# Performance work log

Measured on AMD Instinct MI355X. Metric: run time of the kernel, lower is better.

The kernel has to match this reference:

```python
import jax, jax.numpy as jnp
import numpy as np

EPS = 1e-4      # geomloss: eps = blur**p = 0.01**2
N_ITERS = 20    # fixed Sinkhorn iterations
UNI_T = 2.0     # uniformity temperature (Wang & Isola)


def _sqdist(x, y):
    # [N,D],[M,D] -> [N,M] squared euclidean distances
    return jnp.sum((x[:, None, :] - y[None, :, :]) ** 2, axis=-1)


def _cost(x, y):
    # geomloss p=2 cost: ||x-y||^2 / 2
    return 0.5 * _sqdist(x, y)


def _softmin(C, h):
    # f_i = -eps * log( (1/M) * sum_j exp((h_j - C_ij)/eps) )
    M = C.shape[1]
    lse = jax.nn.logsumexp((h[None, :] - C) / EPS, axis=1)
    return -EPS * (lse - jnp.log(jnp.float32(M)))


def _sinkhorn_potentials(C):
    # alternating log-domain Sinkhorn updates, uniform weights
    def body(carry, _):
        f, g = carry
        f = _softmin(C, g)
        g = _softmin(C.T, f)
        return (f, g), None
    init = (jnp.zeros(C.shape[0], C.dtype), jnp.zeros(C.shape[1], C.dtype))
    (f, g), _ = jax.lax.scan(body, init, None, length=N_ITERS)
    return f, g


def _sym_potential(C):
    # symmetric fixed-point for the debiasing terms OT_eps(a,a)
    def body(p, _):
        return 0.5 * (p + _softmin(C, p)), None
    p, _ = jax.lax.scan(body, jnp.zeros(C.shape[0], C.dtype), None, length=N_ITERS)
    return p


def sinkhorn_divergence(x, y):
    # debiased: S = OT(x,y) - 0.5*OT(x,x) - 0.5*OT(y,y); envelope-theorem grads
    Cxy = _cost(x, y)
    f_d, g_d = _sinkhorn_potentials(jax.lax.stop_gradient(Cxy))
    f = _softmin(Cxy, jax.lax.stop_gradient(g_d))          # final differentiable step
    g = _softmin(Cxy.T, jax.lax.stop_gradient(f_d))

    Cxx = _cost(x, x)
    px = _sym_potential(jax.lax.stop_gradient(Cxx))
    fx = _softmin(Cxx, jax.lax.stop_gradient(px))          # 0.5*OT(x,x) = mean(fx)

    Cyy = _cost(y, y)
    py = _sym_potential(jax.lax.stop_gradient(Cyy))
    fy = _softmin(Cyy, jax.lax.stop_gradient(py))

    return jnp.mean(f) + jnp.mean(g) - jnp.mean(fx) - jnp.mean(fy)


def uniformity(x):
    # log E_{i != j} [ exp(-t * ||x_i - x_j||^2) ]
    N = x.shape[0]
    D = _sqdist(x, x)
    D = D + jnp.diag(jnp.full((N,), jnp.inf, dtype=x.dtype))  # mask self-pairs
    return jax.nn.logsumexp(-UNI_T * D) - jnp.log(jnp.float32(N * (N - 1)))


def setup_inputs() -> dict:
    key = jax.random.key(0)
    k1, k2 = jax.random.split(key)
    p_q = jax.random.normal(k1, (4096, 3), dtype=jnp.float32)
    p_gt = jax.random.normal(k2, (4096, 4), dtype=jnp.float32)
    return {"p_q": p_q, "p_gt": p_gt}


def reference(p_q, p_gt):
    L = sinkhorn_divergence(p_q, p_gt[:, :3])
    L = L + uniformity(p_q)
    return L
```

## Files before the change

kernel.cpp:

```cpp
#include <hip/hip_runtime.h>

#define NPT  4096
#define NBLK 256
#define NTHR 1024

constexpr float EPSV   = 1e-4f;
constexpr float LN2F   = 0.69314718055994531f;
constexpr float E2     = EPSV * LN2F;
constexpr float INV_E2 = 1.0f / E2;
constexpr float S_U    = 4.0f / LN2F;

#define SMEM_FLOATS 34816
#define SMEM_BYTES  (SMEM_FLOATS * 4)

typedef float v2f __attribute__((ext_vector_type(2)));

__device__ __forceinline__ float fexp2(float x) { return __builtin_amdgcn_exp2f(x); }
__device__ __forceinline__ float flog2(float x) { return __builtin_amdgcn_logf(x); }

__device__ __forceinline__ v2f pk_fma(v2f a, v2f b, v2f c) {
    v2f d;
    asm("v_pk_fma_f32 %0, %1, %2, %3" : "=v"(d) : "v"(a), "v"(b), "v"(c));
    return d;
}
__device__ __forceinline__ v2f pk_add(v2f a, v2f b) {
    v2f d;
    asm("v_pk_add_f32 %0, %1, %2" : "=v"(d) : "v"(a), "v"(b));
    return d;
}
__device__ __forceinline__ float max3f(float a, float b, float c) {
    float d;
    asm("v_max3_f32 %0, %1, %2, %3" : "=v"(d) : "v"(a), "v"(b), "v"(c));
    return d;
}

template<int CTRL>
__device__ __forceinline__ float dppf(float x) {
    return __int_as_float(__builtin_amdgcn_update_dpp(
        __float_as_int(x), __float_as_int(x), CTRL, 0xF, 0xF, false));
}

__device__ __forceinline__ float gload(const float* p) {
    return __hip_atomic_load(p, __ATOMIC_RELAXED, __HIP_MEMORY_SCOPE_SYSTEM);
}
__device__ __forceinline__ void gstore(float* p, float v) {
    __hip_atomic_store(p, v, __ATOMIC_RELAXED, __HIP_MEMORY_SCOPE_SYSTEM);
}

__device__ __forceinline__ void group_barrier(unsigned* base, unsigned target, int b) {
    asm volatile("s_waitcnt vmcnt(0)" ::: "memory");
    __syncthreads();
    if (threadIdx.x == 0) {
        __hip_atomic_fetch_add(&base[(b & 15) * 16], 1u,
                               __ATOMIC_RELAXED, __HIP_MEMORY_SCOPE_SYSTEM);
        for (;;) {
            unsigned tot = 0;
#pragma unroll
            for (int i = 0; i < 16; ++i)
                tot += __hip_atomic_load(&base[i * 16],
                                         __ATOMIC_RELAXED, __HIP_MEMORY_SCOPE_SYSTEM);
            if (tot >= target) break;
            __builtin_amdgcn_s_sleep(1);
        }
    }
    __syncthreads();
}

template<bool ISU>
__device__ __forceinline__ void run_task(
    const float4* __restrict__ cpA, const float4* __restrict__ cpB,
    const float*  __restrict__ rAf, const float*  __restrict__ rBf,
    int r0g, int half, int lane, float scale, float2* part2, int lr0)
{
    v2f xs0[2], xs1[2], xs2[2];
#pragma unroll
    for (int r = 0; r < 2; ++r) {
        const int rr = r0g + r;
        const int pb4 = (rr >> 1) * 4, c0 = rr & 1;
        float xv = rAf[pb4 + c0] * scale;
        float yv = rAf[pb4 + 2 + c0] * scale;
        float zv = rBf[pb4 + c0] * scale;
        xs0[r] = (v2f){xv, xv};
        xs1[r] = (v2f){yv, yv};
        xs2[r] = (v2f){zv, zv};
    }
    float m[2], s[2];
    const int pbase = half * 1024 + lane;
    const float4* colA = cpA + pbase;
    const float4* colB = cpB + pbase;

#pragma unroll
    for (int chunk = 0; chunk < 4; ++chunk) {
        v2f av[2][4];
        float mc[2] = {-1e30f, -1e30f};
#pragma unroll
        for (int k = 0; k < 4; ++k) {
            const float4 a4 = colA[(chunk * 4 + k) * 64];
            const float4 b4 = colB[(chunk * 4 + k) * 64];
            const v2f xx = {a4.x, a4.y}, yy = {a4.z, a4.w};
            const v2f zz = {b4.x, b4.y}, gg = {b4.z, b4.w};
#pragma unroll
            for (int r = 0; r < 2; ++r) {
                v2f a01 = pk_fma(xs2[r], zz, gg);
                a01 = pk_fma(xs1[r], yy, a01);
                a01 = pk_fma(xs0[r], xx, a01);
                if (ISU) {
                    const int p = pbase + (chunk * 4 + k) * 64;
                    const int rr = r0g + r;
                    if (p == (rr >> 1)) {
                        if (rr & 1) a01.y = -1e30f; else a01.x = -1e30f;
                    }
                }
                av[r][k] = a01;
                mc[r] = max3f(mc[r], a01.x, a01.y);
            }
        }
#pragma unroll
        for (int r = 0; r < 2; ++r) {
            const float nm = -mc[r];
            v2f mcn = {nm, nm};
            float sA = 0.0f, sB = 0.0f;
#pragma unroll
            for (int k = 0; k < 4; ++k) {
                v2f d = pk_add(av[r][k], mcn);
                sA += fexp2(d.x);
                sB += fexp2(d.y);
            }
            const float sc_ = sA + sB;
            if (chunk == 0) { m[r] = mc[r]; s[r] = sc_; }
            else {
                float dd = m[r] - mc[r];
                float e = fexp2(-fabsf(dd));
                float bigs   = (dd >= 0.0f) ? s[r] : sc_;
                float smalls = (dd >= 0.0f) ? sc_  : s[r];
                s[r] = fmaf(smalls, e, bigs);
                m[r] = fmaxf(m[r], mc[r]);
            }
        }
    }
#pragma unroll
    for (int r = 0; r < 2; ++r) {
        const float ml = m[r];
        float mm = m[r];
        mm = fmaxf(mm, dppf<0xB1>(mm));
        mm = fmaxf(mm, dppf<0x4E>(mm));
        mm = fmaxf(mm, dppf<0x141>(mm));
        float ssv = s[r] * fexp2(ml - mm);
        ssv += dppf<0xB1>(ssv);
        ssv += dppf<0x4E>(ssv);
        ssv += dppf<0x141>(ssv);
        if ((lane & 7) == 0)
            part2[(lr0 + r) * 16 + half * 8 + (lane >> 3)] = make_float2(mm, ssv);
    }
}

__global__ void sink_init(float* __restrict__ ws) {
    int t = blockIdx.x * blockDim.x + threadIdx.x;
    if (t < NPT) {
        gstore(ws + t, 0.0f);
        gstore(ws + 4096 + t, 0.0f);
        gstore(ws + 8192 + t, 0.0f);
        gstore(ws + 16384 + t, 0.0f);
    }
    if (t < 512) {
        __hip_atomic_store((unsigned*)(ws + 40960) + t, 0u,
                           __ATOMIC_RELAXED, __HIP_MEMORY_SCOPE_SYSTEM);
    }
}

__global__ __launch_bounds__(NTHR)
__attribute__((amdgpu_waves_per_eu(4, 4)))
void sink_main(
    const float* __restrict__ xin, const float* __restrict__ yin,
    float* __restrict__ ws, float* __restrict__ out)
{
    extern __shared__ float smem[];
    float4* pAx = (float4*)smem;
    float4* pBx = (float4*)(smem + 8192);
    float4* pAy = (float4*)(smem + 16384);
    float4* pBy = (float4*)(smem + 24576);
    float2* part2 = (float2*)(smem + 32768);

    float* f    = ws;
    float* g    = ws + 4096;
    float* px0  = ws + 8192;
    float* px1  = ws + 12288;
    float* py0  = ws + 16384;
    float* py1  = ws + 20480;
    float* ffin = ws + 24576;
    float* fxv  = ws + 28672;
    float* fyv  = ws + 32768;
    float* uls  = ws + 36864;
    unsigned* ctrA = (unsigned*)(ws + 40960);
    unsigned* ctrB = (unsigned*)(ws + 40960) + 256;

    const int tid  = threadIdx.x;
    const int b    = blockIdx.x;
    const int wave = tid >> 6;
    const int lane = tid & 63;
    unsigned* cbarrier = (b < 128) ? ctrA : ctrB;

    const float4* yin4 = (const float4*)yin;
    for (int i = tid; i < 2048; i += NTHR) {
        float x0 = xin[6 * i + 0], y0v = xin[6 * i + 1], z0 = xin[6 * i + 2];
        float x1 = xin[6 * i + 3], y1v = xin[6 * i + 4], z1 = xin[6 * i + 5];
        pAx[i] = make_float4(x0, x1, y0v, y1v);
        pBx[i] = make_float4(z0, z1, 0.0f, 0.0f);
        float4 v0 = yin4[2 * i], v1 = yin4[2 * i + 1];
        pAy[i] = make_float4(v0.x, v1.x, v0.y, v1.y);
        pBy[i] = make_float4(v0.z, v1.z, 0.0f, 0.0f);
    }
    __syncthreads();

    for (int h = 0; h <= 40; ++h) {
        bool rows_x, cols_x, isU = false, avg = false;
        const float* pot; float* outp; float scale = INV_E2;
        int row0g, rows_pb;
        if (h == 0) {
            if (b < 128)      { rows_x = true;  cols_x = false; pot = g;    outp = f;    rows_pb = 32; row0g = b * 32; }
            else if (b < 192) { rows_x = true;  cols_x = true;  pot = px0;  outp = px1;  avg = true; rows_pb = 64; row0g = (b - 128) * 64; }
            else              { rows_x = true;  cols_x = true;  pot = nullptr; outp = uls; isU = true; scale = S_U; rows_pb = 64; row0g = (b - 192) * 64; }
        } else if (h == 40) {
            if (b < 128)      { rows_x = true;  cols_x = false; pot = g;    outp = ffin; rows_pb = 32; row0g = b * 32; }
            else if (b < 192) { rows_x = true;  cols_x = true;  pot = px0;  outp = fxv;  rows_pb = 64; row0g = (b - 128) * 64; }
            else              { rows_x = false; cols_x = false; pot = py0;  outp = fyv;  rows_pb = 64; row0g = (b - 192) * 64; }
        } else if (h & 1) {
            int k = (h - 1) >> 1;
            if (b < 128) { rows_x = false; cols_x = true;  pot = f; outp = g; rows_pb = 32; row0g = b * 32; }
            else         { rows_x = false; cols_x = false; pot = (k & 1) ? py1 : py0; outp = (k & 1) ? py0 : py1; avg = true; rows_pb = 32; row0g = (b - 128) * 32; }
        } else {
            int k = h >> 1;
            if (b < 128) { rows_x = true; cols_x = false; pot = g; outp = f; rows_pb = 32; row0g = b * 32; }
            else         { rows_x = true; cols_x = true;  pot = (k & 1) ? px1 : px0; outp = (k & 1) ? px0 : px1; avg = true; rows_pb = 32; row0g = (b - 128) * 32; }
        }

        float4* cpA = cols_x ? pAx : pAy;
        float4* cpB = cols_x ? pBx : pBy;
        for (int p = tid; p < 2048; p += NTHR) {
            float4 a4 = cpA[p];
            float4 b4 = cpB[p];
            float cn0 = 0.5f * (a4.x * a4.x + a4.z * a4.z + b4.x * b4.x);
            float cn1 = 0.5f * (a4.y * a4.y + a4.w * a4.w + b4.y * b4.y);
            float pv0 = pot ? gload(pot + 2 * p)     : 0.0f;
            float pv1 = pot ? gload(pot + 2 * p + 1) : 0.0f;
            ((float2*)&cpB[p])[1] = make_float2((pv0 - cn0) * scale,
                                                (pv1 - cn1) * scale);
        }
        __syncthreads();

        const float* rAf = (const float*)(rows_x ? pAx : pAy);
        const float* rBf = (const float*)(rows_x ? pBx : pBy);
        const int ntask = rows_pb;
        for (int t = wave; t < ntask; t += 16) {
            int grp = t >> 1, half = t & 1;
            int lr0 = grp << 1;
            int r0g = row0g + lr0;
            if (isU) run_task<true >(cpA, cpB, rAf, rBf, r0g, half, lane, scale, part2, lr0);
            else     run_task<false>(cpA, cpB, rAf, rBf, r0g, half, lane, scale, part2, lr0);
        }
        __syncthreads();

        if (tid < rows_pb) {
            float2 pv2[16];
#pragma unroll
            for (int q = 0; q < 16; ++q) pv2[q] = part2[tid * 16 + q];
            float mm = pv2[0].x;
#pragma unroll
            for (int q = 1; q < 15; q += 2) mm = max3f(mm, pv2[q].x, pv2[q + 1].x);
            mm = fmaxf(mm, pv2[15].x);
            float ss = 0.0f;
#pragma unroll
            for (int q = 0; q < 16; ++q) ss += pv2[q].y * fexp2(pv2[q].x - mm);
            int rg = row0g + tid;
            const int pb4 = (rg >> 1) * 4, c0 = rg & 1;
            float xv = rAf[pb4 + c0];
            float yv = rAf[pb4 + 2 + c0];
            float zv = rBf[pb4 + c0];
            float rn = 0.5f * (xv * xv + yv * yv + zv * zv);
            float lse2 = mm + flog2(ss) - rn * scale;
            float val;
            if (isU) {
                val = lse2;
            } else {
                val = -E2 * (lse2 - 12.0f);
                if (avg) val = 0.5f * (gload(pot + rg) + val);
            }
            gstore(outp + rg, val);
        }

        group_barrier(cbarrier, 128u * (unsigned)(h + 1), b);
    }

    if (b == 0) {
        if (tid == 0) {
            for (;;) {
                unsigned tot = 0;
#pragma unroll
                for (int i = 0; i < 16; ++i)
                    tot += __hip_atomic_load(&ctrB[i * 16],
                                             __ATOMIC_RELAXED, __HIP_MEMORY_SCOPE_SYSTEM);
                if (tot >= 128u * 41u) break;
                __builtin_amdgcn_s_sleep(1);
            }
        }
        __syncthreads();

        float sf = 0.f, sg = 0.f, sx = 0.f, sy = 0.f, um = -1e30f, us = 0.f;
        for (int i = tid; i < NPT; i += NTHR) {
            sf += gload(ffin + i); sg += gload(g + i);
            sx += gload(fxv + i);  sy += gload(fyv + i);
            float v = gload(uls + i);
            float mn = fmaxf(um, v);
            us = us * fexp2(um - mn) + fexp2(v - mn);
            um = mn;
        }
#pragma unroll
        for (int off = 1; off < 64; off <<= 1) {
            sf += __shfl_xor(sf, off, 64);
            sg += __shfl_xor(sg, off, 64);
            sx += __shfl_xor(sx, off, 64);
            sy += __shfl_xor(sy, off, 64);
            float mo = __shfl_xor(um, off, 64);
            float so = __shfl_xor(us, off, 64);
            float mn = fmaxf(um, mo);
            us = us * fexp2(um - mn) + so * fexp2(mo - mn);
            um = mn;
        }
        __syncthreads();
        if (lane == 0) {
            float* red = smem;
            red[wave * 6 + 0] = sf; red[wave * 6 + 1] = sg; red[wave * 6 + 2] = sx;
            red[wave * 6 + 3] = sy; red[wave * 6 + 4] = um; red[wave * 6 + 5] = us;
        }
        __syncthreads();
        if (tid == 0) {
            float* red = smem;
            float Sf = 0, Sg = 0, Sx = 0, Sy = 0, Um = -1e30f, Us = 0;
            for (int w = 0; w < 16; ++w) {
                Sf += red[w * 6 + 0]; Sg += red[w * 6 + 1];
                Sx += red[w * 6 + 2]; Sy += red[w * 6 + 3];
                float mo = red[w * 6 + 4], so = red[w * 6 + 5];
                float mn = fmaxf(Um, mo);
                Us = Us * fexp2(Um - mn) + so * fexp2(mo - mn);
                Um = mn;
            }
            float mean = (Sf + Sg - Sx - Sy) * (1.0f / 4096.0f);
            float U = LN2F * (Um + flog2(Us)) - logf(4096.0f * 4095.0f);
            out[0] = mean + U;
        }
    }
}

extern "C" void kernel_launch(void* const* d_in, const int* in_sizes, int n_in,
                              void* d_out, int out_size, void* d_ws, size_t ws_size,
                              hipStream_t stream) {
    const float* x = (const float*)d_in[0];
    const float* y = (const float*)d_in[1];
    float* ws  = (float*)d_ws;
    float* out = (float*)d_out;

    (void)hipFuncSetAttribute((const void*)sink_main,
                              hipFuncAttributeMaxDynamicSharedMemorySize, SMEM_BYTES);

    sink_init<<<4, 1024, 0, stream>>>(ws);
    sink_main<<<NBLK, NTHR, SMEM_BYTES, stream>>>(x, y, ws, out);
}
```

Before: 533.8 us.

## Use master-release grid barrier and precompute scaled potentials and norms

Replaces the all-blocks-poll grid barrier with a scheme where block 0 of each group polls the counters and publishes a release flag that the other blocks spin on. Adds precomputed squared norms and pre-scaled potential arrays, written by the init kernel and at each step, so the per-step column staging becomes a single 64-bit load instead of a norm recomputation plus two loads. The row norm in the finalize step is now read from a table. The aim is to cut barrier polling traffic and per-iteration prep latency, at the cost of an extra flag hop in the barrier and extra global stores.

Result: faster. 482.6 us (-9.6%).

```diff
diff --git a/kernel.cpp b/kernel.cpp
--- a/kernel.cpp
+++ b/kernel.cpp
@@ -13,6 +13,27 @@
 #define SMEM_FLOATS 34816
 #define SMEM_BYTES  (SMEM_FLOATS * 4)
 
+#define WF     0
+#define WG     4096
+#define WPX0   8192
+#define WPX1   12288
+#define WPY0   16384
+#define WPY1   20480
+#define WFFIN  24576
+#define WFXV   28672
+#define WFYV   32768
+#define WULS   36864
+#define WCTR   40960
+#define WREL   41472
+#define WCNX   41984
+#define WCNY   46080
+#define WFG    50176
+#define WGG    54272
+#define WPXG0  58368
+#define WPXG1  62464
+#define WPYG0  66560
+#define WPYG1  70656
+
 typedef float v2f __attribute__((ext_vector_type(2)));
 
 __device__ __forceinline__ float fexp2(float x) { return __builtin_amdgcn_exp2f(x); }
@@ -46,21 +67,34 @@
 __device__ __forceinline__ void gstore(float* p, float v) {
     __hip_atomic_store(p, v, __ATOMIC_RELAXED, __HIP_MEMORY_SCOPE_SYSTEM);
 }
-
-__device__ __forceinline__ void group_barrier(unsigned* base, unsigned target, int b) {
+__device__ __forceinline__ float2 gload2(const float* p) {
+    unsigned long long raw = __hip_atomic_load((const unsigned long long*)p,
+                                               __ATOMIC_RELAXED, __HIP_MEMORY_SCOPE_SYSTEM);
+    union { unsigned long long u; float2 f2; } cv; cv.u = raw;
+    return cv.f2;
+}
+
+__device__ __forceinline__ void group_barrier(unsigned* ctr, unsigned* rel,
+                                              unsigned tcnt, unsigned trel, int bb) {
     asm volatile("s_waitcnt vmcnt(0)" ::: "memory");
     __syncthreads();
     if (threadIdx.x == 0) {
-        __hip_atomic_fetch_add(&base[(b & 15) * 16], 1u,
+        __hip_atomic_fetch_add(&ctr[(bb & 15) * 16], 1u,
                                __ATOMIC_RELAXED, __HIP_MEMORY_SCOPE_SYSTEM);
-        for (;;) {
-            unsigned tot = 0;
-#pragma unroll
-            for (int i = 0; i < 16; ++i)
-                tot += __hip_atomic_load(&base[i * 16],
-                                         __ATOMIC_RELAXED, __HIP_MEMORY_SCOPE_SYSTEM);
-            if (tot >= target) break;
-            __builtin_amdgcn_s_sleep(1);
+        if (bb == 0) {
+            for (;;) {
+                unsigned tot = 0;
+#pragma unroll
+                for (int i = 0; i < 16; ++i)
+                    tot += __hip_atomic_load(&ctr[i * 16],
+                                             __ATOMIC_RELAXED, __HIP_MEMORY_SCOPE_SYSTEM);
+                if (tot >= tcnt) break;
+                __builtin_amdgcn_s_sleep(1);
+            }
+            __hip_atomic_store(rel, trel, __ATOMIC_RELAXED, __HIP_MEMORY_SCOPE_SYSTEM);
+        } else {
+            while (__hip_atomic_load(rel, __ATOMIC_RELAXED, __HIP_MEMORY_SCOPE_SYSTEM) < trel)
+                __builtin_amdgcn_s_sleep(1);
         }
     }
     __syncthreads();
@@ -154,16 +188,26 @@
     }
 }
 
-__global__ void sink_init(float* __restrict__ ws) {
+__global__ void sink_init(const float* __restrict__ xin, const float* __restrict__ yin,
+                          float* __restrict__ ws) {
     int t = blockIdx.x * blockDim.x + threadIdx.x;
     if (t < NPT) {
-        gstore(ws + t, 0.0f);
-        gstore(ws + 4096 + t, 0.0f);
-        gstore(ws + 8192 + t, 0.0f);
-        gstore(ws + 16384 + t, 0.0f);
-    }
-    if (t < 512) {
-        __hip_atomic_store((unsigned*)(ws + 40960) + t, 0u,
+        gstore(ws + WF + t, 0.0f);
+        gstore(ws + WG + t, 0.0f);
+        gstore(ws + WPX0 + t, 0.0f);
+        gstore(ws + WPY0 + t, 0.0f);
+        float x0 = xin[3 * t], y0 = xin[3 * t + 1], z0 = xin[3 * t + 2];
+        float cnx = 0.5f * (x0 * x0 + y0 * y0 + z0 * z0);
+        float4 v = ((const float4*)yin)[t];
+        float cny = 0.5f * (v.x * v.x + v.y * v.y + v.z * v.z);
+        ws[WCNX + t] = cnx;
+        ws[WCNY + t] = cny;
+        gstore(ws + WGG   + t, -cny * INV_E2);
+        gstore(ws + WPXG0 + t, -cnx * INV_E2);
+        gstore(ws + WPYG0 + t, -cny * INV_E2);
+    }
+    if (t < 640) {
+        __hip_atomic_store((unsigned*)(ws + WCTR) + t, 0u,
                            __ATOMIC_RELAXED, __HIP_MEMORY_SCOPE_SYSTEM);
     }
 }
@@ -181,24 +225,37 @@
     float4* pBy = (float4*)(smem + 24576);
     float2* part2 = (float2*)(smem + 32768);
 
-    float* f    = ws;
-    float* g    = ws + 4096;
-    float* px0  = ws + 8192;
-    float* px1  = ws + 12288;
-    float* py0  = ws + 16384;
-    float* py1  = ws + 20480;
-    float* ffin = ws + 24576;
-    float* fxv  = ws + 28672;
-    float* fyv  = ws + 32768;
-    float* uls  = ws + 36864;
-    unsigned* ctrA = (unsigned*)(ws + 40960);
-    unsigned* ctrB = (unsigned*)(ws + 40960) + 256;
+    float* f    = ws + WF;
+    float* g    = ws + WG;
+    float* px0  = ws + WPX0;
+    float* px1  = ws + WPX1;
+    float* py0  = ws + WPY0;
+    float* py1  = ws + WPY1;
+    float* ffin = ws + WFFIN;
+    float* fxv  = ws + WFXV;
+    float* fyv  = ws + WFYV;
+    float* uls  = ws + WULS;
+    unsigned* ctrA = (unsigned*)(ws + WCTR);
+    unsigned* ctrB = (unsigned*)(ws + WCTR) + 256;
+    unsigned* relA = (unsigned*)(ws + WREL);
+    unsigned* relB = (unsigned*)(ws + WREL) + 64;
+    const float* cnx = ws + WCNX;
+    const float* cny = ws + WCNY;
+    float* fG   = ws + WFG;
+    float* gG   = ws + WGG;
+    float* pxG0 = ws + WPXG0;
+    float* pxG1 = ws + WPXG1;
+    float* pyG0 = ws + WPYG0;
+    float* pyG1 = ws + WPYG1;
 
     const int tid  = threadIdx.x;
     const int b    = blockIdx.x;
     const int wave = tid >> 6;
     const int lane = tid & 63;
-    unsigned* cbarrier = (b < 128) ? ctrA : ctrB;
+    const bool isA = b < 128;
+    const int bb   = isA ? b : b - 128;
+    unsigned* cctr = isA ? ctrA : ctrB;
+    unsigned* crel = isA ? relA : relB;
 
     const float4* yin4 = (const float4*)yin;
     for (int i = tid; i < 2048; i += NTHR) {
@@ -214,37 +271,45 @@
 
     for (int h = 0; h <= 40; ++h) {
         bool rows_x, cols_x, isU = false, avg = false;
-        const float* pot; float* outp; float scale = INV_E2;
+        const float* pot; const float* potG; float* outp; float* outpG;
+        float scale = INV_E2;
         int row0g, rows_pb;
         if (h == 0) {
-            if (b < 128)      { rows_x = true;  cols_x = false; pot = g;    outp = f;    rows_pb = 32; row0g = b * 32; }
-            else if (b < 192) { rows_x = true;  cols_x = true;  pot = px0;  outp = px1;  avg = true; rows_pb = 64; row0g = (b - 128) * 64; }
-            else              { rows_x = true;  cols_x = true;  pot = nullptr; outp = uls; isU = true; scale = S_U; rows_pb = 64; row0g = (b - 192) * 64; }
+            if (b < 128)      { rows_x = true;  cols_x = false; pot = g;   potG = gG;   outp = f;   outpG = fG;   rows_pb = 32; row0g = b * 32; }
+            else if (b < 192) { rows_x = true;  cols_x = true;  pot = px0; potG = pxG0; outp = px1; outpG = pxG1; avg = true; rows_pb = 64; row0g = (b - 128) * 64; }
+            else              { rows_x = true;  cols_x = true;  pot = nullptr; potG = nullptr; outp = uls; outpG = nullptr; isU = true; scale = S_U; rows_pb = 64; row0g = (b - 192) * 64; }
         } else if (h == 40) {
-            if (b < 128)      { rows_x = true;  cols_x = false; pot = g;    outp = ffin; rows_pb = 32; row0g = b * 32; }
-            else if (b < 192) { rows_x = true;  cols_x = true;  pot = px0;  outp = fxv;  rows_pb = 64; row0g = (b - 128) * 64; }
-            else              { rows_x = false; cols_x = false; pot = py0;  outp = fyv;  rows_pb = 64; row0g = (b - 192) * 64; }
+            if (b < 128)      { rows_x = true;  cols_x = false; pot = g;   potG = gG;   outp = ffin; outpG = nullptr; rows_pb = 32; row0g = b * 32; }
+            else if (b < 192) { rows_x = true;  cols_x = true;  pot = px0; potG = pxG0; outp = fxv;  outpG = nullptr; rows_pb = 64; row0g = (b - 128) * 64; }
+            else              { rows_x = false; cols_x = false; pot = py0; potG = pyG0; outp = fyv;  outpG = nullptr; rows_pb = 64; row0g = (b - 192) * 64; }
         } else if (h & 1) {
             int k = (h - 1) >> 1;
-            if (b < 128) { rows_x = false; cols_x = true;  pot = f; outp = g; rows_pb = 32; row0g = b * 32; }
-            else         { rows_x = false; cols_x = false; pot = (k & 1) ? py1 : py0; outp = (k & 1) ? py0 : py1; avg = true; rows_pb = 32; row0g = (b - 128) * 32; }
+            if (b < 128) { rows_x = false; cols_x = true;  pot = f; potG = fG; outp = g; outpG = gG; rows_pb = 32; row0g = b * 32; }
+            else         { rows_x = false; cols_x = false;
+                           pot  = (k & 1) ? py1  : py0;  potG  = (k & 1) ? pyG1 : pyG0;
+                           outp = (k & 1) ? py0  : py1;  outpG = (k & 1) ? pyG0 : pyG1;
+                           avg = true; rows_pb = 32; row0g = (b - 128) * 32; }
         } else {
             int k = h >> 1;
-            if (b < 128) { rows_x = true; cols_x = false; pot = g; outp = f; rows_pb = 32; row0g = b * 32; }
-            else         { rows_x = true; cols_x = true;  pot = (k & 1) ? px1 : px0; outp = (k & 1) ? px0 : px1; avg = true; rows_pb = 32; row0g = (b - 128) * 32; }
+            if (b < 128) { rows_x = true; cols_x = false; pot = g; potG = gG; outp = f; outpG = fG; rows_pb = 32; row0g = b * 32; }
+            else         { rows_x = true; cols_x = true;
+                           pot  = (k & 1) ? px1  : px0;  potG  = (k & 1) ? pxG1 : pxG0;
+                           outp = (k & 1) ? px0  : px1;  outpG = (k & 1) ? pxG0 : pxG1;
+                           avg = true; rows_pb = 32; row0g = (b - 128) * 32; }
         }
 
         float4* cpA = cols_x ? pAx : pAy;
         float4* cpB = cols_x ? pBx : pBy;
+        const float* ccn = cols_x ? cnx : cny;
         for (int p = tid; p < 2048; p += NTHR) {
-            float4 a4 = cpA[p];
-            float4 b4 = cpB[p];
-            float cn0 = 0.5f * (a4.x * a4.x + a4.z * a4.z + b4.x * b4.x);
-            float cn1 = 0.5f * (a4.y * a4.y + a4.w * a4.w + b4.y * b4.y);
-            float pv0 = pot ? gload(pot + 2 * p)     : 0.0f;
-            float pv1 = pot ? gload(pot + 2 * p + 1) : 0.0f;
-            ((float2*)&cpB[p])[1] = make_float2((pv0 - cn0) * scale,
-                                                (pv1 - cn1) * scale);
+            float2 g2;
+            if (isU) {
+                float2 cn2 = ((const float2*)ccn)[p];
+                g2 = make_float2(-cn2.x * S_U, -cn2.y * S_U);
+            } else {
+                g2 = gload2(potG + 2 * p);
+            }
+            ((float2*)&cpB[p])[1] = g2;
         }
         __syncthreads();
 
@@ -260,6 +325,7 @@
         }
         __syncthreads();
 
+        const float* rcn = rows_x ? cnx : cny;
         if (tid < rows_pb) {
             float2 pv2[16];
 #pragma unroll
@@ -272,11 +338,7 @@
 #pragma unroll
             for (int q = 0; q < 16; ++q) ss += pv2[q].y * fexp2(pv2[q].x - mm);
             int rg = row0g + tid;
-            const int pb4 = (rg >> 1) * 4, c0 = rg & 1;
-            float xv = rAf[pb4 + c0];
-            float yv = rAf[pb4 + 2 + c0];
-            float zv = rBf[pb4 + c0];
-            float rn = 0.5f * (xv * xv + yv * yv + zv * zv);
+            float rn = rcn[rg];
             float lse2 = mm + flog2(ss) - rn * scale;
             float val;
             if (isU) {
@@ -286,22 +348,16 @@
                 if (avg) val = 0.5f * (gload(pot + rg) + val);
             }
             gstore(outp + rg, val);
-        }
-
-        group_barrier(cbarrier, 128u * (unsigned)(h + 1), b);
+            if (outpG) gstore(outpG + rg, (val - rn) * INV_E2);
+        }
+
+        group_barrier(cctr, crel, 128u * (unsigned)(h + 1), (unsigned)(h + 1), bb);
     }
 
     if (b == 0) {
         if (tid == 0) {
-            for (;;) {
-                unsigned tot = 0;
-#pragma unroll
-                for (int i = 0; i < 16; ++i)
-                    tot += __hip_atomic_load(&ctrB[i * 16],
-                                             __ATOMIC_RELAXED, __HIP_MEMORY_SCOPE_SYSTEM);
-                if (tot >= 128u * 41u) break;
+            while (__hip_atomic_load(relB, __ATOMIC_RELAXED, __HIP_MEMORY_SCOPE_SYSTEM) < 41u)
                 __builtin_amdgcn_s_sleep(1);
-            }
         }
         __syncthreads();
 
@@ -362,6 +418,6 @@
     (void)hipFuncSetAttribute((const void*)sink_main,
                               hipFuncAttributeMaxDynamicSharedMemorySize, SMEM_BYTES);
 
-    sink_init<<<4, 1024, 0, stream>>>(ws);
+    sink_init<<<4, 1024, 0, stream>>>(x, y, ws);
     sink_main<<<NBLK, NTHR, SMEM_BYTES, stream>>>(x, y, ws, out);
 }
```
